# Kernel tuning notes

Measured on AMD Instinct MI355X. Metric: run time of the kernel, lower is better.

## Reference

```python
import jax, jax.numpy as jnp
from jax import lax
import numpy as np

B, L, D = 4, 4096, 1024
H = 16
HD = D // H          # 64
WIN = 256
NC = L // WIN
N_ITER = 50          # entmax-bisect iterations (entmax library default)
LN_EPS = 1e-5


def _p(x, am1):
    # clamp(x, min=0) ** (1/(alpha-1))
    return jnp.clip(x, 0.0) ** (1.0 / am1)


def entmax_bisect(X, alpha):
    """alpha-entmax along the last axis via bisection. alpha broadcastable to X."""
    am1 = alpha - 1.0
    Xs = X * am1
    d = X.shape[-1]
    max_val = Xs.max(axis=-1, keepdims=True)
    tau_lo = max_val - 1.0                       # 1 ** (alpha-1)
    tau_hi = max_val - (1.0 / d) ** am1
    f_lo = _p(Xs - tau_lo, am1).sum(-1, keepdims=True) - 1.0
    dm0 = tau_hi - tau_lo

    def body(i, carry):
        tau_lo, dm, _ = carry
        dm = dm * 0.5
        tau_m = tau_lo + dm
        f_m = _p(Xs - tau_m, am1).sum(-1, keepdims=True) - 1.0
        tau_lo = jnp.where(f_m * f_lo >= 0, tau_m, tau_lo)
        return (tau_lo, dm, tau_m)

    tau_lo, dm, tau_m = lax.fori_loop(0, N_ITER, body, (tau_lo, dm0, tau_lo))
    p = _p(Xs - tau_m, am1)
    return p / p.sum(-1, keepdims=True)          # ensure_sum_one


def setup_inputs() -> dict:
    key = jax.random.key(0)
    ks = jax.random.split(key, 4)
    x = jax.random.normal(ks[0], (B, L, D), jnp.float32)
    alpha = jnp.full((H,), 1.5, jnp.float32)
    qkv_w = 0.02 * jax.random.normal(ks[1], (3 * D, D), jnp.float32)
    qkv_b = jnp.zeros((3 * D,), jnp.float32)
    o_w = 0.02 * jax.random.normal(ks[2], (D, D), jnp.float32)
    o_b = jnp.zeros((D,), jnp.float32)
    ln_gamma = jnp.ones((D,), jnp.float32)
    ln_beta = jnp.zeros((D,), jnp.float32)
    return {"x": x, "alpha": alpha, "qkv_w": qkv_w, "qkv_b": qkv_b,
            "o_w": o_w, "o_b": o_b, "ln_gamma": ln_gamma, "ln_beta": ln_beta}


def reference(x, alpha, qkv_w, qkv_b, o_w, o_b, ln_gamma, ln_beta):
    # qkv projection -> [B, H, L, 3*HD]
    qkv = (x @ qkv_w.T + qkv_b).reshape(B, L, H, 3 * HD).transpose(0, 2, 1, 3)
    q, k, v = jnp.split(qkv, 3, axis=-1)
    # block-diagonal windows (span=None => k/v chunks coincide with q chunks)
    qc = q.reshape(B, H, NC, WIN, HD)
    kc = k.reshape(B, H, NC, WIN, HD)
    vc = v.reshape(B, H, NC, WIN, HD)
    scores = jnp.einsum('bhcqd,bhckd->bhcqk', qc, kc) / np.sqrt(HD).astype(np.float32)
    weights = entmax_bisect(scores, alpha.reshape(1, H, 1, 1, 1))
    out = jnp.einsum('bhcqk,bhckd->bhcqd', weights, vc)
    out = out.reshape(B, H, L, HD).transpose(0, 2, 1, 3).reshape(B, L, D)
    # layer norm
    mu = out.mean(-1, keepdims=True)
    var = out.var(-1, keepdims=True)
    out = (out - mu) * lax.rsqrt(var + LN_EPS) * ln_gamma + ln_beta
    return out @ o_w.T + o_b
```

## Files before the change

### kernel.cpp

```cpp
#include <hip/hip_runtime.h>

typedef unsigned short u16;
typedef unsigned int   u32;
typedef __attribute__((ext_vector_type(8))) short bf16x8;
typedef __attribute__((ext_vector_type(4))) float f32x4;
typedef __attribute__((ext_vector_type(8))) u16  u16x8;

__device__ __forceinline__ float b2f(u16 u) {
    union { u32 i; float f; } v; v.i = ((u32)u) << 16; return v.f;
}
__device__ __forceinline__ u16 f2b(float f) {
    u32 i = __float_as_uint(f);
    u32 r = (i + 0x7FFFu + ((i >> 16) & 1u)) >> 16;
    return (u16)r;
}
__device__ __forceinline__ bool is_bf16(const u32* gprobe) { return *gprobe == 0x3F803F80u; }

__device__ __forceinline__ void load_lds16(const void* g, void* l) {
    __builtin_amdgcn_global_load_lds((__attribute__((address_space(1))) void*)g,
                                     (__attribute__((address_space(3))) void*)l, 16, 0, 0);
}

__global__ __launch_bounds__(256) void cvt_kern(const void* __restrict__ src, u16* __restrict__ dst,
                                                int n8, const u32* __restrict__ gprobe) {
    const bool isb = is_bf16(gprobe);
    const int i = blockIdx.x * 256 + threadIdx.x;
    if (i >= n8) return;
    if (isb) {
        ((u16x8*)dst)[i] = ((const u16x8*)src)[i];
    } else {
        const float* s = (const float*)src + (size_t)i * 8;
        u16x8 o;
        #pragma unroll
        for (int j = 0; j < 8; j++) o[j] = f2b(s[j]);
        ((u16x8*)dst)[i] = o;
    }
}

__global__ __launch_bounds__(256) void gemm_bt(const u16* __restrict__ A, const u16* __restrict__ B,
                                               const void* __restrict__ bias,
                                               u16* __restrict__ Cb, float* __restrict__ Cf,
                                               const u32* __restrict__ gprobe, int out_mode,
                                               int M, int N, int K) {
    __shared__ u16 lsA[128 * 32];
    __shared__ u16 lsB[128 * 32];
    const int tid  = threadIdx.x;
    const int wave = tid >> 6, lane = tid & 63;
    const int m0 = blockIdx.y * 128, n0 = blockIdx.x * 128;
    const int wr = wave >> 1, wc = wave & 1;

    f32x4 acc[4][4] = {};

    const int srow = wave * 16 + (lane >> 2);
    const int scol = (lane & 3) * 8;
    const u16* gA0 = A + (size_t)(m0 + srow) * K + scol;
    const u16* gB0 = B + (size_t)(n0 + srow) * K + scol;
    u16* lA0 = &lsA[wave * 512];
    u16* lB0 = &lsB[wave * 512];
    const size_t rstep = (size_t)64 * K;

    for (int k0 = 0; k0 < K; k0 += 32) {
        __syncthreads();
        load_lds16(gA0 + k0,         lA0);
        load_lds16(gA0 + k0 + rstep, lA0 + 2048);
        load_lds16(gB0 + k0,         lB0);
        load_lds16(gB0 + k0 + rstep, lB0 + 2048);
        __syncthreads();

        bf16x8 af[4], bfr[4];
        #pragma unroll
        for (int mi = 0; mi < 4; mi++)
            af[mi] = *(const bf16x8*)&lsA[(wr * 64 + mi * 16 + (lane & 15)) * 32 + (lane >> 4) * 8];
        #pragma unroll
        for (int ni = 0; ni < 4; ni++)
            bfr[ni] = *(const bf16x8*)&lsB[(wc * 64 + ni * 16 + (lane & 15)) * 32 + (lane >> 4) * 8];
        #pragma unroll
        for (int mi = 0; mi < 4; mi++)
            #pragma unroll
            for (int ni = 0; ni < 4; ni++)
                acc[mi][ni] = __builtin_amdgcn_mfma_f32_16x16x32_bf16(af[mi], bfr[ni], acc[mi][ni], 0, 0, 0);
    }

    const bool isb     = is_bf16(gprobe);
    const bool store_b = (out_mode == 0) || isb;
    const int g = lane >> 4, cc = lane & 15;
    #pragma unroll
    for (int ni = 0; ni < 4; ni++) {
        const int col = n0 + wc * 64 + ni * 16 + cc;
        const float bv = isb ? b2f(((const u16*)bias)[col]) : ((const float*)bias)[col];
        #pragma unroll
        for (int mi = 0; mi < 4; mi++) {
            const int row = m0 + wr * 64 + mi * 16 + g * 4;
            #pragma unroll
            for (int i = 0; i < 4; i++) {
                const float v = acc[mi][ni][i] + bv;
                const size_t idx = (size_t)(row + i) * N + col;
                if (store_b) Cb[idx] = f2b(v);
                else         Cf[idx] = v;
            }
        }
    }
}

__device__ __forceinline__ void bfly_sum4(float (&a)[4]) {
    #pragma unroll
    for (int m = 1; m <= 8; m <<= 1)
        #pragma unroll
        for (int i = 0; i < 4; i++) a[i] += __shfl_xor(a[i], m, 64);
}

__device__ __forceinline__ void entmax2_rows(f32x4 (&s)[16]) {
    float mx[4] = {-3e38f, -3e38f, -3e38f, -3e38f};
    #pragma unroll
    for (int nt = 0; nt < 16; nt++)
        #pragma unroll
        for (int i = 0; i < 4; i++) mx[i] = fmaxf(mx[i], s[nt][i]);
    #pragma unroll
    for (int m = 1; m <= 8; m <<= 1)
        #pragma unroll
        for (int i = 0; i < 4; i++) mx[i] = fmaxf(mx[i], __shfl_xor(mx[i], m, 64));

    float tau[4];
    #pragma unroll
    for (int i = 0; i < 4; i++) tau[i] = mx[i] - 1.0f;

    #pragma unroll 1
    for (int it = 0; it < 10; it++) {
        float a2[4] = {0.f, 0.f, 0.f, 0.f};
        float a1[4] = {0.f, 0.f, 0.f, 0.f};
        #pragma unroll
        for (int nt = 0; nt < 16; nt++)
            #pragma unroll
            for (int i = 0; i < 4; i++) {
                float t = fmaxf(s[nt][i] - tau[i], 0.0f);
                a2[i] = fmaf(t, t, a2[i]);
                a1[i] += t;
            }
        bfly_sum4(a2);
        bfly_sum4(a1);
        #pragma unroll
        for (int i = 0; i < 4; i++)
            tau[i] += (a2[i] - 1.0f) * 0.5f * __builtin_amdgcn_rcpf(a1[i]);
    }

    float ss[4] = {0.f, 0.f, 0.f, 0.f};
    #pragma unroll
    for (int nt = 0; nt < 16; nt++)
        #pragma unroll
        for (int i = 0; i < 4; i++) {
            float t = fmaxf(s[nt][i] - tau[i], 0.0f);
            float p = t * t;
            s[nt][i] = p;
            ss[i] += p;
        }
    bfly_sum4(ss);
    float inv[4];
    #pragma unroll
    for (int i = 0; i < 4; i++) inv[i] = 1.0f / ss[i];
    #pragma unroll
    for (int nt = 0; nt < 16; nt++)
        #pragma unroll
        for (int i = 0; i < 4; i++) s[nt][i] *= inv[i];
}

__device__ __forceinline__ void entmax_gen_rows(f32x4 (&s)[16], float e, float dm0) {
    float mx[4] = {-3e38f, -3e38f, -3e38f, -3e38f};
    #pragma unroll
    for (int nt = 0; nt < 16; nt++)
        #pragma unroll
        for (int i = 0; i < 4; i++) mx[i] = fmaxf(mx[i], s[nt][i]);
    #pragma unroll
    for (int m = 1; m <= 8; m <<= 1)
        #pragma unroll
        for (int i = 0; i < 4; i++) mx[i] = fmaxf(mx[i], __shfl_xor(mx[i], m, 64));

    float tau_lo[4], tau_m[4], f_lo[4];
    #pragma unroll
    for (int i = 0; i < 4; i++) { tau_lo[i] = mx[i] - 1.0f; tau_m[i] = tau_lo[i]; }
    {
        float a[4] = {0.f, 0.f, 0.f, 0.f};
        #pragma unroll
        for (int nt = 0; nt < 16; nt++)
            #pragma unroll
            for (int i = 0; i < 4; i++) {
                float t = fmaxf(s[nt][i] - tau_lo[i], 0.0f);
                a[i] += (t > 0.0f) ? __expf(e * __logf(t)) : 0.0f;
            }
        bfly_sum4(a);
        #pragma unroll
        for (int i = 0; i < 4; i++) f_lo[i] = a[i] - 1.0f;
    }
    float dm = dm0;
    #pragma unroll 1
    for (int it = 0; it < 26; it++) {
        dm *= 0.5f;
        #pragma unroll
        for (int i = 0; i < 4; i++) tau_m[i] = tau_lo[i] + dm;
        float a[4] = {0.f, 0.f, 0.f, 0.f};
        #pragma unroll
        for (int nt = 0; nt < 16; nt++)
            #pragma unroll
            for (int i = 0; i < 4; i++) {
                float t = fmaxf(s[nt][i] - tau_m[i], 0.0f);
                a[i] += (t > 0.0f) ? __expf(e * __logf(t)) : 0.0f;
            }
        bfly_sum4(a);
        #pragma unroll
        for (int i = 0; i < 4; i++)
            tau_lo[i] = ((a[i] - 1.0f) * f_lo[i] >= 0.0f) ? tau_m[i] : tau_lo[i];
    }
    float ss[4] = {0.f, 0.f, 0.f, 0.f};
    #pragma unroll
    for (int nt = 0; nt < 16; nt++)
        #pragma unroll
        for (int i = 0; i < 4; i++) {
            float t = fmaxf(s[nt][i] - tau_m[i], 0.0f);
            float p = (t > 0.0f) ? __expf(e * __logf(t)) : 0.0f;
            s[nt][i] = p;
            ss[i] += p;
        }
    bfly_sum4(ss);
    float inv[4];
    #pragma unroll
    for (int i = 0; i < 4; i++) inv[i] = 1.0f / ss[i];
    #pragma unroll
    for (int nt = 0; nt < 16; nt++)
        #pragma unroll
        for (int i = 0; i < 4; i++) s[nt][i] *= inv[i];
}

__global__ __launch_bounds__(256, 4) void attn_win(const u16* __restrict__ qkv,
                                                   const void* __restrict__ alpha, u16* __restrict__ att,
                                                   const u32* __restrict__ gprobe) {
    __shared__ u16 Vt[64 * 264];
    __shared__ u16 Wl[4 * 16 * 40];
    const int tid  = threadIdx.x;
    const int wave = tid >> 6, lane = tid & 63;
    const int c = blockIdx.x, h = blockIdx.y, b = blockIdx.z;
    const int g = lane >> 4, cc = lane & 15;

    const float av  = is_bf16(gprobe) ? b2f(((const u16*)alpha)[h]) : ((const float*)alpha)[h];
    const float am1 = av - 1.0f;
    const float e   = 1.0f / am1;
    const bool  sq  = (e == 2.0f);
    const float scl = am1 * 0.125f;
    const float dm0 = 1.0f - exp2f(-8.0f * am1);

    const size_t tok0 = (size_t)b * 4096 + (size_t)c * 256;
    const u16* qbase = qkv + tok0 * 3072 + h * 192;
    const u16* kbase = qbase + 64;
    const u16* vbase = qbase + 128;
    u16* wl = &Wl[wave * (16 * 40)];

    {
        const int d = tid & 63, tg = tid >> 6;
        #pragma unroll
        for (int j = 0; j < 8; j++) {
            const int t0 = tg * 64 + j * 8;
            u16x8 tmp;
            #pragma unroll
            for (int i = 0; i < 8; i++)
                tmp[i] = vbase[(size_t)(t0 + i) * 3072 + d];
            *(u16x8*)&Vt[d * 264 + t0] = tmp;
        }
    }
    __syncthreads();

    for (int ch = 0; ch < 4; ch++) {
        const int r0 = ch * 64 + wave * 16;

        const u16* qr = qbase + (size_t)(r0 + cc) * 3072 + g * 8;
        bf16x8 aq0 = *(const bf16x8*)qr;
        bf16x8 aq1 = *(const bf16x8*)(qr + 32);

        f32x4 s[16] = {};
        #pragma unroll
        for (int nt = 0; nt < 16; nt++) {
            const u16* kr = kbase + (size_t)(nt * 16 + cc) * 3072 + g * 8;
            bf16x8 bk0 = *(const bf16x8*)kr;
            bf16x8 bk1 = *(const bf16x8*)(kr + 32);
            s[nt] = __builtin_amdgcn_mfma_f32_16x16x32_bf16(aq0, bk0, s[nt], 0, 0, 0);
            s[nt] = __builtin_amdgcn_mfma_f32_16x16x32_bf16(aq1, bk1, s[nt], 0, 0, 0);
        }
        #pragma unroll
        for (int nt = 0; nt < 16; nt++)
            #pragma unroll
            for (int i = 0; i < 4; i++) s[nt][i] *= scl;

        if (sq) entmax2_rows(s);
        else    entmax_gen_rows(s, e, dm0);

        f32x4 o[4] = {};
        #pragma unroll
        for (int kc = 0; kc < 8; kc++) {
            #pragma unroll
            for (int t = 0; t < 2; t++) {
                const int nt = kc * 2 + t;
                #pragma unroll
                for (int i = 0; i < 4; i++)
                    wl[(g * 4 + i) * 40 + t * 16 + cc] = f2b(s[nt][i]);
            }
            bf16x8 aw = *(const bf16x8*)&wl[cc * 40 + g * 8];
            #pragma unroll
            for (int nd = 0; nd < 4; nd++) {
                bf16x8 bv = *(const bf16x8*)&Vt[(nd * 16 + cc) * 264 + kc * 32 + g * 8];
                o[nd] = __builtin_amdgcn_mfma_f32_16x16x32_bf16(aw, bv, o[nd], 0, 0, 0);
            }
        }

        u16* ob = att + (tok0 + r0) * 1024 + h * 64;
        #pragma unroll
        for (int nd = 0; nd < 4; nd++)
            #pragma unroll
            for (int i = 0; i < 4; i++)
                ob[(size_t)(g * 4 + i) * 1024 + nd * 16 + cc] = f2b(o[nd][i]);
    }
}

__global__ __launch_bounds__(256) void ln_kern(const u16* __restrict__ att, const void* __restrict__ gam,
                                               const void* __restrict__ bet, u16* __restrict__ out,
                                               const u32* __restrict__ gprobe) {
    const bool isb = is_bf16(gprobe);
    const int tid = threadIdx.x;
    const int wave = tid >> 6, lane = tid & 63;
    const size_t tok = (size_t)blockIdx.x * 4 + wave;
    const u16* p = att + tok * 1024 + lane * 16;
    u16x8 v0 = *(const u16x8*)p;
    u16x8 v1 = *(const u16x8*)(p + 8);
    float x[16];
    #pragma unroll
    for (int j = 0; j < 8; j++) { x[j] = b2f(v0[j]); x[j + 8] = b2f(v1[j]); }
    float s = 0.f, s2 = 0.f;
    #pragma unroll
    for (int j = 0; j < 16; j++) { s += x[j]; s2 = fmaf(x[j], x[j], s2); }
    #pragma unroll
    for (int m = 1; m <= 32; m <<= 1) { s += __shfl_xor(s, m, 64); s2 += __shfl_xor(s2, m, 64); }
    const float mean = s * (1.0f / 1024.0f);
    const float var  = s2 * (1.0f / 1024.0f) - mean * mean;
    const float rs   = rsqrtf(var + 1e-5f);

    float gv[16], bv[16];
    if (isb) {
        const u16* gp = (const u16*)gam + lane * 16;
        const u16* bp = (const u16*)bet + lane * 16;
        u16x8 g0 = *(const u16x8*)gp, g1 = *(const u16x8*)(gp + 8);
        u16x8 b0 = *(const u16x8*)bp, b1 = *(const u16x8*)(bp + 8);
        #pragma unroll
        for (int j = 0; j < 8; j++) {
            gv[j] = b2f(g0[j]); gv[j + 8] = b2f(g1[j]);
            bv[j] = b2f(b0[j]); bv[j + 8] = b2f(b1[j]);
        }
    } else {
        const float* gp = (const float*)gam + lane * 16;
        const float* bp = (const float*)bet + lane * 16;
        #pragma unroll
        for (int j = 0; j < 16; j++) { gv[j] = gp[j]; bv[j] = bp[j]; }
    }

    u16x8 w0, w1;
    #pragma unroll
    for (int j = 0; j < 8; j++) {
        w0[j] = f2b((x[j]     - mean) * rs * gv[j]     + bv[j]);
        w1[j] = f2b((x[j + 8] - mean) * rs * gv[j + 8] + bv[j + 8]);
    }
    u16* op = out + tok * 1024 + lane * 16;
    *(u16x8*)op       = w0;
    *(u16x8*)(op + 8) = w1;
}

extern "C" void kernel_launch(void* const* d_in, const int* in_sizes, int n_in,
                              void* d_out, int out_size, void* d_ws, size_t ws_size,
                              hipStream_t stream) {
    const void* x      = d_in[0];
    const void* alpha  = d_in[1];
    const void* qkv_w  = d_in[2];
    const void* qkv_b  = d_in[3];
    const void* o_w    = d_in[4];
    const void* o_b    = d_in[5];
    const u32*  gprobe = (const u32*)d_in[6];
    const void* gam    = d_in[6];
    const void* bet    = d_in[7];

    u16* xb  = (u16*)d_ws;
    u16* wq  = xb + (size_t)16384 * 1024;
    u16* wo  = wq + (size_t)3072 * 1024;
    u16* qkv = wo + (size_t)1024 * 1024;
    u16* att = (u16*)d_out;
    u16* ln  = xb;

    dim3 blk(256);
    cvt_kern<<<dim3((16384 * 1024 / 8 + 255) / 256), blk, 0, stream>>>(x, xb, 16384 * 1024 / 8, gprobe);
    cvt_kern<<<dim3((3072 * 1024 / 8 + 255) / 256), blk, 0, stream>>>(qkv_w, wq, 3072 * 1024 / 8, gprobe);
    cvt_kern<<<dim3((1024 * 1024 / 8 + 255) / 256), blk, 0, stream>>>(o_w, wo, 1024 * 1024 / 8, gprobe);
    gemm_bt<<<dim3(3072 / 128, 16384 / 128), blk, 0, stream>>>(xb, wq, qkv_b, qkv, nullptr, gprobe, 0,
                                                               16384, 3072, 1024);
    attn_win<<<dim3(16, 16, 4), blk, 0, stream>>>(qkv, alpha, att, gprobe);
    ln_kern<<<dim3(4096), blk, 0, stream>>>(att, gam, bet, ln, gprobe);
    gemm_bt<<<dim3(1024 / 128, 16384 / 128), blk, 0, stream>>>(ln, wo, o_b, (u16*)d_out, (float*)d_out,
                                                               gprobe, 1, 16384, 1024, 1024);
}
```

Baseline: 617.6 us.

## Stage K in LDS, prefetch next Q chunk, and coalesce output stores

The attention-window kernel now copies the 256x64 K tile into shared memory once per block instead of reloading it from global memory for every 16-row chunk. The Q fragments for the next chunk are prefetched while the current one is computed. Output tiles are staged through the per-wave LDS buffer and written as 16-byte vectors instead of scattered 2-byte stores. The larger shared-memory footprint is why the occupancy hint in launch bounds drops from 4 to 2 blocks, which may reduce latency hiding during the long entmax bisection.

```diff
diff --git a/kernel.cpp b/kernel.cpp
--- a/kernel.cpp
+++ b/kernel.cpp
@@ -229,11 +229,12 @@
         for (int i = 0; i < 4; i++) s[nt][i] *= inv[i];
 }
 
-__global__ __launch_bounds__(256, 4) void attn_win(const u16* __restrict__ qkv,
+__global__ __launch_bounds__(256, 2) void attn_win(const u16* __restrict__ qkv,
                                                    const void* __restrict__ alpha, u16* __restrict__ att,
                                                    const u32* __restrict__ gprobe) {
     __shared__ u16 Vt[64 * 264];
-    __shared__ u16 Wl[4 * 16 * 40];
+    __shared__ u16 Kl[256 * 72];
+    __shared__ u16 Wl[4 * 16 * 72];
     const int tid  = threadIdx.x;
     const int wave = tid >> 6, lane = tid & 63;
     const int c = blockIdx.x, h = blockIdx.y, b = blockIdx.z;
@@ -250,7 +251,17 @@
     const u16* qbase = qkv + tok0 * 3072 + h * 192;
     const u16* kbase = qbase + 64;
     const u16* vbase = qbase + 128;
-    u16* wl = &Wl[wave * (16 * 40)];
+    u16* wl = &Wl[wave * (16 * 72)];
+
+    {
+        const int kr = tid >> 3, kc2 = tid & 7;
+        #pragma unroll
+        for (int it = 0; it < 8; it++) {
+            const int row = it * 32 + kr;
+            bf16x8 kv = *(const bf16x8*)(kbase + (size_t)row * 3072 + kc2 * 8);
+            *(bf16x8*)&Kl[row * 72 + kc2 * 8] = kv;
+        }
+    }
 
     {
         const int d = tid & 63, tg = tid >> 6;
@@ -266,21 +277,32 @@
     }
     __syncthreads();
 
+    bf16x8 q0, q1;
+    {
+        const u16* qr = qbase + (size_t)(wave * 16 + cc) * 3072 + g * 8;
+        q0 = *(const bf16x8*)qr;
+        q1 = *(const bf16x8*)(qr + 32);
+    }
+
     for (int ch = 0; ch < 4; ch++) {
         const int r0 = ch * 64 + wave * 16;
 
-        const u16* qr = qbase + (size_t)(r0 + cc) * 3072 + g * 8;
-        bf16x8 aq0 = *(const bf16x8*)qr;
-        bf16x8 aq1 = *(const bf16x8*)(qr + 32);
+        bf16x8 n0, n1;
+        {
+            const int chn = (ch + 1) & 3;
+            const u16* qr = qbase + (size_t)(chn * 64 + wave * 16 + cc) * 3072 + g * 8;
+            n0 = *(const bf16x8*)qr;
+            n1 = *(const bf16x8*)(qr + 32);
+        }
 
         f32x4 s[16] = {};
         #pragma unroll
         for (int nt = 0; nt < 16; nt++) {
-            const u16* kr = kbase + (size_t)(nt * 16 + cc) * 3072 + g * 8;
-            bf16x8 bk0 = *(const bf16x8*)kr;
-            bf16x8 bk1 = *(const bf16x8*)(kr + 32);
-            s[nt] = __builtin_amdgcn_mfma_f32_16x16x32_bf16(aq0, bk0, s[nt], 0, 0, 0);
-            s[nt] = __builtin_amdgcn_mfma_f32_16x16x32_bf16(aq1, bk1, s[nt], 0, 0, 0);
+            const u16* krow = &Kl[(nt * 16 + cc) * 72 + g * 8];
+            bf16x8 bk0 = *(const bf16x8*)krow;
+            bf16x8 bk1 = *(const bf16x8*)(krow + 32);
+            s[nt] = __builtin_amdgcn_mfma_f32_16x16x32_bf16(q0, bk0, s[nt], 0, 0, 0);
+            s[nt] = __builtin_amdgcn_mfma_f32_16x16x32_bf16(q1, bk1, s[nt], 0, 0, 0);
         }
         #pragma unroll
         for (int nt = 0; nt < 16; nt++)
@@ -308,12 +330,19 @@
             }
         }
 
-        u16* ob = att + (tok0 + r0) * 1024 + h * 64;
         #pragma unroll
         for (int nd = 0; nd < 4; nd++)
             #pragma unroll
             for (int i = 0; i < 4; i++)
-                ob[(size_t)(g * 4 + i) * 1024 + nd * 16 + cc] = f2b(o[nd][i]);
+                wl[(g * 4 + i) * 72 + nd * 16 + cc] = f2b(o[nd][i]);
+        #pragma unroll
+        for (int p = 0; p < 2; p++) {
+            const int row = p * 8 + (lane >> 3);
+            u16x8 val = *(const u16x8*)&wl[row * 72 + (lane & 7) * 8];
+            *(u16x8*)(att + (size_t)(tok0 + r0 + row) * 1024 + h * 64 + (lane & 7) * 8) = val;
+        }
+
+        q0 = n0; q1 = n1;
     }
 }
 
```

Measured after the change: 536.8 us. 1.15x faster.
